# Performance work log

Hardware: AMD Instinct MI355X
Metric: run time of the kernel (lower is better)

Reference implementation:

```python
import jax, jax.numpy as jnp
import numpy as np

N_CODES = 1024
CODE_DIM = 64
COMMITMENT_WEIGHT = 0.5
DECAY = 0.99
EPSILON = 1e-05
TEMP = 1.0


def setup_inputs() -> dict:
    key = jax.random.key(0)
    k_z, k_e = jax.random.split(key)
    z = jax.random.normal(k_z, (8, 16384, CODE_DIM), dtype=jnp.float32)
    # xavier_uniform init for embedding [n_codes, code_dim]
    limit = float(np.sqrt(6.0 / (N_CODES + CODE_DIM)))
    embedding = jax.random.uniform(k_e, (N_CODES, CODE_DIM), dtype=jnp.float32,
                                   minval=-limit, maxval=limit)
    ema_cluster_size = jnp.zeros((N_CODES,), dtype=jnp.float32)
    ema_w = embedding.copy()
    return {"z": z, "embedding": embedding,
            "ema_cluster_size": ema_cluster_size, "ema_w": ema_w}


def reference(z, embedding, ema_cluster_size, ema_w):
    lead_shape = z.shape[:-1]
    zf = z.reshape(-1, z.shape[-1])  # [N, D]
    # squared-euclidean distances: ||z||^2 + ||e||^2 - 2 z e^T  -> [N, n_codes]
    d = (jnp.sum(zf * zf, axis=-1, keepdims=True)
         + jnp.sum(embedding * embedding, axis=-1)
         - 2.0 * (zf @ embedding.T)) / TEMP
    idx = jnp.argmin(d, axis=-1)  # [N]
    z_q_f = embedding[idx]        # [N, D]

    # --- EMA codebook update (no-grad buffer math) ---
    ones = jnp.ones_like(idx, dtype=zf.dtype)
    cluster_size = jax.ops.segment_sum(ones, idx, num_segments=N_CODES)      # one_hot.sum(0)
    new_ecs = ema_cluster_size * DECAY + (1.0 - DECAY) * cluster_size
    n = jnp.sum(new_ecs)
    cs = jnp.clip((new_ecs + EPSILON) / (n + N_CODES * EPSILON) * n, 0.01)
    dw = jax.ops.segment_sum(zf, idx, num_segments=N_CODES)                  # one_hot.T @ z
    new_ema_w = ema_w * DECAY + (1.0 - DECAY) * dw
    new_embedding = new_ema_w / cs[:, None]

    # --- losses (straight-through) ---
    z_q = z_q_f.reshape(z.shape)
    commitment_loss = jnp.mean((jax.lax.stop_gradient(z_q) - z) ** 2)
    codebook_loss = jnp.mean((z_q - jax.lax.stop_gradient(z)) ** 2)
    loss = commitment_loss * COMMITMENT_WEIGHT + codebook_loss
    z_q_st = z + jax.lax.stop_gradient(z_q - z)

    # --- perplexity (no-grad) ---
    avg_probs = cluster_size / jnp.sum(cluster_size)
    avg_probs = jnp.clip(avg_probs, 1e-10)
    avg_probs = avg_probs / jnp.sum(avg_probs)
    perplexity = jnp.exp(-jnp.sum(avg_probs * jnp.log(avg_probs)))

    encoding_indices = idx.reshape(lead_shape)
    return (z_q_st, encoding_indices, loss, perplexity,
            new_embedding, new_ecs, new_ema_w)
```

## Files before the change

kernel.cpp:

```cpp
#include <hip/hip_runtime.h>
#include <hip/hip_bf16.h>
#include <math.h>

#define N_ROWS   131072
#define DIMS     64
#define NCODES   1024
#define DECAY    0.99f
#define EPSF     1e-5f
#define BAND     2e-3f

#define OFF_ZQ    0
#define OFF_IDX   8388608
#define OFF_LOSS  8519680
#define OFF_PERP  8519681
#define OFF_EMB   8519682
#define OFF_ECS   8585218
#define OFF_EMAW  8586242

typedef unsigned int uint;
typedef short bf16x8 __attribute__((ext_vector_type(8)));
typedef float f32x4  __attribute__((ext_vector_type(4)));

__device__ __forceinline__ float atomic_add_f32(float* p, float v) {
  return __hip_atomic_fetch_add(p, v, __ATOMIC_RELAXED, __HIP_MEMORY_SCOPE_AGENT);
}

__device__ __forceinline__ unsigned short bf16_rne(float f) {
  uint u = __float_as_uint(f);
  uint r = u + 0x7fffu + ((u >> 16) & 1u);
  return (unsigned short)(r >> 16);
}
__device__ __forceinline__ float bf16_f32(unsigned short h) {
  return __uint_as_float(((uint)h) << 16);
}

__device__ __forceinline__ float np_pairwise64_sq(const float* v) {
#pragma clang fp contract(off)
  float r[8];
#pragma unroll
  for (int j = 0; j < 8; ++j) r[j] = v[j] * v[j];
#pragma unroll
  for (int i = 8; i < 64; i += 8)
#pragma unroll
    for (int j = 0; j < 8; ++j) r[j] += v[i + j] * v[i + j];
  return ((r[0] + r[1]) + (r[2] + r[3])) + ((r[4] + r[5]) + (r[6] + r[7]));
}

__global__ __launch_bounds__(256) void k0m(const float* __restrict__ emb,
                                           float* __restrict__ ee,
                                           uint* __restrict__ cluster,
                                           uint* __restrict__ cnt,
                                           bf16x8* __restrict__ bsplit,
                                           float* __restrict__ dw) {
  int T = blockIdx.x;
  int t = threadIdx.x;
  int gid = T * 256 + t;
  for (int i = gid; i < NCODES * DIMS; i += 16384) dw[i] = 0.0f;

  int l = t & 63;
  int slot = t >> 6;
  int ktile = slot >> 1, split = slot & 1;
  int code = T * 16 + (l & 15);
  int k0 = ktile * 32 + ((l >> 4) << 3);
  const float* ep = emb + (size_t)code * DIMS + k0;
  float4 fa = *(const float4*)ep;
  float4 fb = *(const float4*)(ep + 4);
  float fs[8] = {fa.x, fa.y, fa.z, fa.w, fb.x, fb.y, fb.z, fb.w};
  bf16x8 v;
#pragma unroll
  for (int i = 0; i < 8; ++i) {
    unsigned short h = bf16_rne(fs[i]);
    if (split == 0) v[i] = (short)h;
    else            v[i] = (short)bf16_rne(fs[i] - bf16_f32(h));
  }
  bsplit[(size_t)((T * 2 + ktile) * 2 + split) * 64 + l] = v;

  if (t < 16) {
    int c = T * 16 + t;
    float ev[DIMS];
    const float4* e4 = (const float4*)(emb + (size_t)c * DIMS);
#pragma unroll
    for (int i = 0; i < 16; ++i) {
      float4 w = e4[i];
      ev[4*i] = w.x; ev[4*i+1] = w.y; ev[4*i+2] = w.z; ev[4*i+3] = w.w;
    }
    ee[c] = np_pairwise64_sq(ev);
  } else if (t < 32) {
    cluster[T * 16 + (t - 16)] = 0u;
  }
  if (T == 0 && t == 32) *cnt = 0u;
}

__global__ __launch_bounds__(256) void k1_mfma(const float* __restrict__ z,
                                               const bf16x8* __restrict__ bsplit,
                                               const float* __restrict__ ee,
                                               int* __restrict__ idx_out,
                                               float* __restrict__ idx_f_out,
                                               uint* __restrict__ cluster,
                                               uint* __restrict__ cnt,
                                               uint* __restrict__ list) {
  __shared__ bf16x8 btile[4 * 64];
  __shared__ float  eel[NCODES];
  int t = threadIdx.x;
  int l = t & 63;
  int w = t >> 6;
  int rowbase = blockIdx.x * 64 + w * 16;
  int arow = rowbase + (l & 15);
  int kq = (l >> 4) << 3;
  int col = l & 15;

  for (int i = t; i < NCODES; i += 256) eel[i] = ee[i];

  bf16x8 ahi[2], ami[2];
#pragma unroll
  for (int t2 = 0; t2 < 2; ++t2) {
    const float* zp = z + (size_t)arow * DIMS + t2 * 32 + kq;
    float4 fa = *(const float4*)zp;
    float4 fb = *(const float4*)(zp + 4);
    float fs[8] = {fa.x, fa.y, fa.z, fa.w, fb.x, fb.y, fb.z, fb.w};
#pragma unroll
    for (int i = 0; i < 8; ++i) {
      unsigned short h = bf16_rne(fs[i]);
      float m = fs[i] - bf16_f32(h);
      ahi[t2][i] = (short)bf16_rne(-2.0f * fs[i]);
      ami[t2][i] = (short)bf16_rne(-2.0f * m);
    }
  }

  float best[4]  = {3.4e38f, 3.4e38f, 3.4e38f, 3.4e38f};
  float second[4] = {3.4e38f, 3.4e38f, 3.4e38f, 3.4e38f};
  int   bidx[4] = {0, 0, 0, 0};

  bf16x8 vpre = bsplit[(size_t)(0 * 4 + w) * 64 + l];

  for (int T = 0; T < 64; ++T) {
    __syncthreads();
    btile[w * 64 + l] = vpre;
    if (T < 63) vpre = bsplit[(size_t)((T + 1) * 4 + w) * 64 + l];
    __syncthreads();

    int code = T * 16 + col;
    float eeT = eel[code];
    bf16x8 bhi0 = btile[0 * 64 + l];
    bf16x8 bmi0 = btile[1 * 64 + l];
    bf16x8 bhi1 = btile[2 * 64 + l];
    bf16x8 bmi1 = btile[3 * 64 + l];

    f32x4 acc = {eeT, eeT, eeT, eeT};
    acc = __builtin_amdgcn_mfma_f32_16x16x32_bf16(ahi[0], bhi0, acc, 0, 0, 0);
    acc = __builtin_amdgcn_mfma_f32_16x16x32_bf16(ahi[1], bhi1, acc, 0, 0, 0);
    acc = __builtin_amdgcn_mfma_f32_16x16x32_bf16(ahi[0], bmi0, acc, 0, 0, 0);
    acc = __builtin_amdgcn_mfma_f32_16x16x32_bf16(ahi[1], bmi1, acc, 0, 0, 0);
    acc = __builtin_amdgcn_mfma_f32_16x16x32_bf16(ami[0], bhi0, acc, 0, 0, 0);
    acc = __builtin_amdgcn_mfma_f32_16x16x32_bf16(ami[1], bhi1, acc, 0, 0, 0);

#pragma unroll
    for (int j = 0; j < 4; ++j) {
      float s = acc[j];
      bool lt = s < best[j];
      second[j] = lt ? best[j] : fminf(second[j], s);
      best[j]   = lt ? s : best[j];
      bidx[j]   = lt ? code : bidx[j];
    }
  }

#pragma unroll
  for (int m = 1; m < 16; m <<= 1) {
#pragma unroll
    for (int j = 0; j < 4; ++j) {
      float ob = __shfl_xor(best[j], m, 64);
      float os = __shfl_xor(second[j], m, 64);
      int   oi = __shfl_xor(bidx[j], m, 64);
      if (ob < best[j]) {
        second[j] = fminf(os, best[j]);
        best[j] = ob; bidx[j] = oi;
      } else if (ob == best[j]) {
        bidx[j] = min(bidx[j], oi);
        second[j] = fminf(second[j], fminf(os, ob));
      } else {
        second[j] = fminf(second[j], ob);
      }
    }
  }

  if (col == 0) {
#pragma unroll
    for (int j = 0; j < 4; ++j) {
      int r = rowbase + ((l >> 4) << 2) + j;
      idx_out[r] = bidx[j];
      idx_f_out[r] = (float)bidx[j];
      atomicAdd(&cluster[bidx[j]], 1u);
      if (second[j] - best[j] < BAND) {
        uint p = atomicAdd(cnt, 1u);
        list[p] = (uint)r;
      }
    }
  }
}

__global__ __launch_bounds__(256) void k2_recheck(const float* __restrict__ z,
                                                  const float* __restrict__ emb,
                                                  const float* __restrict__ ee,
                                                  const uint* __restrict__ cnt,
                                                  const uint* __restrict__ list,
                                                  int* __restrict__ idx_out,
                                                  float* __restrict__ idx_f_out,
                                                  uint* __restrict__ cluster) {
#pragma clang fp contract(off)
  __shared__ float zrow[DIMS];
  __shared__ float rv[256];
  __shared__ int   ri[256];
  int t = threadIdx.x;
  uint n = *cnt;
  for (uint i = blockIdx.x; i < n; i += gridDim.x) {
    uint row = list[i];
    __syncthreads();
    if (t < 16)
      ((float4*)zrow)[t] = ((const float4*)(z + (size_t)row * DIMS))[t];
    __syncthreads();
    float zz = np_pairwise64_sq(zrow);
    float best = 3.4e38f; int bi = 0;
#pragma unroll
    for (int k4 = 0; k4 < 4; ++k4) {
      int c = t * 4 + k4;
      const float* e = emb + (size_t)c * DIMS;
      float a = 0.f;
      for (int k = 0; k < DIMS; ++k) a = fmaf(zrow[k], e[k], a);
      float d = fmaf(-2.0f, a, zz + ee[c]);
      if (d < best) { best = d; bi = c; }
    }
    rv[t] = best; ri[t] = bi;
    __syncthreads();
    for (int s = 128; s > 0; s >>= 1) {
      if (t < s) {
        float ov = rv[t + s]; int oi = ri[t + s];
        if (ov < rv[t] || (ov == rv[t] && oi < ri[t])) { rv[t] = ov; ri[t] = oi; }
      }
      __syncthreads();
    }
    if (t == 0) {
      int old = idx_out[row];
      if (ri[0] != old) {
        atomicSub(&cluster[old], 1u);
        atomicAdd(&cluster[ri[0]], 1u);
        idx_out[row] = ri[0];
        idx_f_out[row] = (float)ri[0];
      }
    }
  }
}

__global__ __launch_bounds__(256) void kp(const uint* __restrict__ cluster,
                                          const float* __restrict__ ecs_in,
                                          uint* __restrict__ starts,
                                          uint* __restrict__ cursor,
                                          float* __restrict__ csb,
                                          float* __restrict__ out) {
  __shared__ uint a[256], b[256];
  __shared__ double red[256];
  int t = threadIdx.x;

  uint c0 = cluster[t*4+0], c1 = cluster[t*4+1], c2 = cluster[t*4+2], c3 = cluster[t*4+3];
  uint s4 = c0 + c1 + c2 + c3;
  a[t] = s4;
  __syncthreads();
  uint* src = a; uint* dst = b;
  for (int off = 1; off < 256; off <<= 1) {
    dst[t] = src[t] + ((t >= off) ? src[t - off] : 0u);
    __syncthreads();
    uint* tmp = src; src = dst; dst = tmp;
  }
  uint base = (t > 0) ? src[t-1] : 0u;
  uint p0 = base, p1 = p0 + c0, p2 = p1 + c1, p3 = p2 + c2;
  starts[t*4+0] = p0; starts[t*4+1] = p1; starts[t*4+2] = p2; starts[t*4+3] = p3;
  cursor[t*4+0] = p0; cursor[t*4+1] = p1; cursor[t*4+2] = p2; cursor[t*4+3] = p3;
  if (t == 255) starts[NCODES] = src[255];
  __syncthreads();

  double nloc = 0.0, aloc = 0.0, bloc = 0.0;
  for (int c = t; c < NCODES; c += 256) {
    float cntf = (float)cluster[c];
    float ne = ecs_in[c] * DECAY + (1.0f - DECAY) * cntf;
    out[OFF_ECS + c] = ne;
    nloc += (double)ne;
    double p = (double)cntf / (double)N_ROWS;
    double pc = p < 1e-10 ? 1e-10 : p;
    bloc += pc;
    aloc += pc * log(pc);
  }

  red[t] = nloc; __syncthreads();
  for (int s = 128; s > 0; s >>= 1) { if (t < s) red[t] += red[t + s]; __syncthreads(); }
  double n = red[0]; __syncthreads();

  red[t] = bloc; __syncthreads();
  for (int s = 128; s > 0; s >>= 1) { if (t < s) red[t] += red[t + s]; __syncthreads(); }
  double B = red[0]; __syncthreads();

  red[t] = aloc; __syncthreads();
  for (int s = 128; s > 0; s >>= 1) { if (t < s) red[t] += red[t + s]; __syncthreads(); }
  double A = red[0]; __syncthreads();

  if (t == 0) {
    double ent = -(A / B - log(B));
    out[OFF_PERP] = (float)exp(ent);
  }

  float nf = (float)n;
  for (int c = t; c < NCODES; c += 256) {
    float ne = out[OFF_ECS + c];
    float cs = ((ne + EPSF) / (nf + (float)NCODES * EPSF)) * nf;
    csb[c] = cs < 0.01f ? 0.01f : cs;
  }
}

__global__ __launch_bounds__(256) void k3c_scatter(const int* __restrict__ idx,
                                                   uint* __restrict__ cursor,
                                                   uint* __restrict__ rowids,
                                                   int* __restrict__ codes) {
  int row = blockIdx.x * 256 + threadIdx.x;
  int code = idx[row];
  uint pos = atomicAdd(&cursor[code], 1u);
  rowids[pos] = (uint)row;
  codes[pos] = code;
}

__global__ __launch_bounds__(256) void k3d_fused(const float* __restrict__ z,
                                                 const float* __restrict__ emb,
                                                 const uint* __restrict__ rowids,
                                                 const int* __restrict__ codes,
                                                 float* __restrict__ out_zq,
                                                 float* __restrict__ dw,
                                                 double* __restrict__ sqpart) {
  __shared__ double accd[4];
  int lane = threadIdx.x & 63, w = threadIdx.x >> 6;
  int base = blockIdx.x * 128 + w * 32;

  int cur = codes[base];
  float acc = 0.f;
  double ds = 0.0;
  for (int i = 0; i < 32; ++i) {
    int p = base + i;
    uint r = rowids[p];
    int c = codes[p];
    if (c != cur) {
      atomic_add_f32(&dw[cur * DIMS + lane], acc);
      acc = 0.f; cur = c;
    }
    float zv = z[(size_t)r * DIMS + lane];
    float ev = emb[c * DIMS + lane];
    float d = ev - zv;
    float o = zv + d;
    out_zq[(size_t)r * DIMS + lane] = o;
    acc += zv;
    ds += (double)(d * d);
  }
  atomic_add_f32(&dw[cur * DIMS + lane], acc);

#pragma unroll
  for (int o2 = 32; o2 > 0; o2 >>= 1) ds += __shfl_down(ds, o2, 64);
  if (lane == 0) accd[w] = ds;
  __syncthreads();
  if (threadIdx.x == 0)
    sqpart[blockIdx.x] = (accd[0] + accd[1]) + (accd[2] + accd[3]);
}

__global__ __launch_bounds__(256) void k4b_emb(const float* __restrict__ emaw_in,
                                               const float* __restrict__ dw,
                                               const float* __restrict__ csb,
                                               const double* __restrict__ sqpart,
                                               float* __restrict__ out) {
  int i = blockIdx.x * 256 + threadIdx.x;
  int c = i >> 6;
  float nw = emaw_in[i] * DECAY + (1.0f - DECAY) * dw[i];
  out[OFF_EMAW + i] = nw;
  out[OFF_EMB + i] = nw / csb[c];

  if (blockIdx.x == 0) {
    __shared__ double red[256];
    int t = threadIdx.x;
    double sloc = 0.0;
    for (int k = t; k < 1024; k += 256) sloc += sqpart[k];
    red[t] = sloc; __syncthreads();
    for (int s = 128; s > 0; s >>= 1) { if (t < s) red[t] += red[t + s]; __syncthreads(); }
    if (t == 0) {
      double M = red[0] / (double)((size_t)N_ROWS * DIMS);
      out[OFF_LOSS] = (float)(1.5 * M);
    }
  }
}

extern "C" void kernel_launch(void* const* d_in, const int* in_sizes, int n_in,
                              void* d_out, int out_size, void* d_ws, size_t ws_size,
                              hipStream_t stream) {
  const float* z    = (const float*)d_in[0];
  const float* emb  = (const float*)d_in[1];
  const float* ecs  = (const float*)d_in[2];
  const float* emaw = (const float*)d_in[3];
  float* out = (float*)d_out;

  char* ws = (char*)d_ws;
  uint*   cnt    = (uint*)   (ws + 0);
  int*    idxw   = (int*)    (ws + 16);
  uint*   clus   = (uint*)   (ws + 524304);
  float*  dw     = (float*)  (ws + 528416);
  float*  ee     = (float*)  (ws + 790560);
  float*  csb    = (float*)  (ws + 794656);
  uint*   starts = (uint*)   (ws + 798752);
  uint*   cursor = (uint*)   (ws + 806944);
  uint*   rowids = (uint*)   (ws + 811040);
  bf16x8* bsplit = (bf16x8*) (ws + 1335328);
  uint*   rlist  = (uint*)   (ws + 1597472);
  double* sqpart = (double*) (ws + 1597472);
  int*    codes  = (int*)    (ws + 2121760);

  k0m<<<64, 256, 0, stream>>>(emb, ee, clus, cnt, bsplit, dw);
  k1_mfma<<<N_ROWS / 64, 256, 0, stream>>>(z, bsplit, ee, idxw, out + OFF_IDX,
                                           clus, cnt, rlist);
  k2_recheck<<<1024, 256, 0, stream>>>(z, emb, ee, cnt, rlist, idxw,
                                       out + OFF_IDX, clus);
  kp<<<1, 256, 0, stream>>>(clus, ecs, starts, cursor, csb, out);
  k3c_scatter<<<N_ROWS / 256, 256, 0, stream>>>(idxw, cursor, rowids, codes);
  k3d_fused<<<N_ROWS / 128, 256, 0, stream>>>(z, emb, rowids, codes,
                                              out + OFF_ZQ, dw, sqpart);
  k4b_emb<<<256, 256, 0, stream>>>(emaw, dw, csb, sqpart, out);
}
```

Measured before the change: 195.4 us.

## Fuse z_q output and loss partials into the MFMA argmin kernel

Moves the straight-through z_q write and the squared-error loss partial sums out of the sorted-order dw kernel and into the argmin kernel, where z rows are read coalesced by block. Rows whose index changes during the exact recheck get their z_q rewritten and a loss correction term recorded, which the final kernel adds back in. The dw kernel now only gathers z. The argmin loop also stages two code tiles per barrier pair, halving the number of synchronisations. This removes the scattered z_q writes but adds an extra z read in the argmin kernel and a correction path.

```diff
diff --git a/kernel.cpp b/kernel.cpp
--- a/kernel.cpp
+++ b/kernel.cpp
@@ -92,15 +92,20 @@
 }
 
 __global__ __launch_bounds__(256) void k1_mfma(const float* __restrict__ z,
+                                               const float* __restrict__ emb,
                                                const bf16x8* __restrict__ bsplit,
                                                const float* __restrict__ ee,
                                                int* __restrict__ idx_out,
                                                float* __restrict__ idx_f_out,
+                                               float* __restrict__ out_zq,
+                                               double* __restrict__ sqpart,
                                                uint* __restrict__ cluster,
                                                uint* __restrict__ cnt,
                                                uint* __restrict__ list) {
-  __shared__ bf16x8 btile[4 * 64];
+  __shared__ bf16x8 btile[2][256];
   __shared__ float  eel[NCODES];
+  __shared__ int    sidx[64];
+  __shared__ double wred[4];
   int t = threadIdx.x;
   int l = t & 63;
   int w = t >> 6;
@@ -131,36 +136,44 @@
   float second[4] = {3.4e38f, 3.4e38f, 3.4e38f, 3.4e38f};
   int   bidx[4] = {0, 0, 0, 0};
 
-  bf16x8 vpre = bsplit[(size_t)(0 * 4 + w) * 64 + l];
-
-  for (int T = 0; T < 64; ++T) {
-    __syncthreads();
-    btile[w * 64 + l] = vpre;
-    if (T < 63) vpre = bsplit[(size_t)((T + 1) * 4 + w) * 64 + l];
-    __syncthreads();
-
-    int code = T * 16 + col;
-    float eeT = eel[code];
-    bf16x8 bhi0 = btile[0 * 64 + l];
-    bf16x8 bmi0 = btile[1 * 64 + l];
-    bf16x8 bhi1 = btile[2 * 64 + l];
-    bf16x8 bmi1 = btile[3 * 64 + l];
-
-    f32x4 acc = {eeT, eeT, eeT, eeT};
-    acc = __builtin_amdgcn_mfma_f32_16x16x32_bf16(ahi[0], bhi0, acc, 0, 0, 0);
-    acc = __builtin_amdgcn_mfma_f32_16x16x32_bf16(ahi[1], bhi1, acc, 0, 0, 0);
-    acc = __builtin_amdgcn_mfma_f32_16x16x32_bf16(ahi[0], bmi0, acc, 0, 0, 0);
-    acc = __builtin_amdgcn_mfma_f32_16x16x32_bf16(ahi[1], bmi1, acc, 0, 0, 0);
-    acc = __builtin_amdgcn_mfma_f32_16x16x32_bf16(ami[0], bhi0, acc, 0, 0, 0);
-    acc = __builtin_amdgcn_mfma_f32_16x16x32_bf16(ami[1], bhi1, acc, 0, 0, 0);
-
-#pragma unroll
-    for (int j = 0; j < 4; ++j) {
-      float s = acc[j];
-      bool lt = s < best[j];
-      second[j] = lt ? best[j] : fminf(second[j], s);
-      best[j]   = lt ? s : best[j];
-      bidx[j]   = lt ? code : bidx[j];
+  bf16x8 vp0 = bsplit[(size_t)(0 * 4 + w) * 64 + l];
+  bf16x8 vp1 = bsplit[(size_t)(1 * 4 + w) * 64 + l];
+
+  for (int T = 0; T < 64; T += 2) {
+    __syncthreads();
+    btile[0][w * 64 + l] = vp0;
+    btile[1][w * 64 + l] = vp1;
+    __syncthreads();
+    if (T + 2 < 64) {
+      vp0 = bsplit[(size_t)((T + 2) * 4 + w) * 64 + l];
+      vp1 = bsplit[(size_t)((T + 3) * 4 + w) * 64 + l];
+    }
+
+#pragma unroll
+    for (int u = 0; u < 2; ++u) {
+      int code = (T + u) * 16 + col;
+      float eeT = eel[code];
+      bf16x8 bhi0 = btile[u][0 * 64 + l];
+      bf16x8 bmi0 = btile[u][1 * 64 + l];
+      bf16x8 bhi1 = btile[u][2 * 64 + l];
+      bf16x8 bmi1 = btile[u][3 * 64 + l];
+
+      f32x4 acc = {eeT, eeT, eeT, eeT};
+      acc = __builtin_amdgcn_mfma_f32_16x16x32_bf16(ahi[0], bhi0, acc, 0, 0, 0);
+      acc = __builtin_amdgcn_mfma_f32_16x16x32_bf16(ahi[1], bhi1, acc, 0, 0, 0);
+      acc = __builtin_amdgcn_mfma_f32_16x16x32_bf16(ahi[0], bmi0, acc, 0, 0, 0);
+      acc = __builtin_amdgcn_mfma_f32_16x16x32_bf16(ahi[1], bmi1, acc, 0, 0, 0);
+      acc = __builtin_amdgcn_mfma_f32_16x16x32_bf16(ami[0], bhi0, acc, 0, 0, 0);
+      acc = __builtin_amdgcn_mfma_f32_16x16x32_bf16(ami[1], bhi1, acc, 0, 0, 0);
+
+#pragma unroll
+      for (int j = 0; j < 4; ++j) {
+        float s = acc[j];
+        bool lt = s < best[j];
+        second[j] = lt ? best[j] : fminf(second[j], s);
+        best[j]   = lt ? s : best[j];
+        bidx[j]   = lt ? code : bidx[j];
+      }
     }
   }
 
@@ -186,7 +199,9 @@
   if (col == 0) {
 #pragma unroll
     for (int j = 0; j < 4; ++j) {
-      int r = rowbase + ((l >> 4) << 2) + j;
+      int lrow = w * 16 + ((l >> 4) << 2) + j;
+      int r = blockIdx.x * 64 + lrow;
+      sidx[lrow] = bidx[j];
       idx_out[r] = bidx[j];
       idx_f_out[r] = (float)bidx[j];
       atomicAdd(&cluster[bidx[j]], 1u);
@@ -196,6 +211,32 @@
       }
     }
   }
+  __syncthreads();
+
+  double ds = 0.0;
+  const float4* z4 = (const float4*)z;
+  const float4* e4 = (const float4*)emb;
+  float4* zq4 = (float4*)out_zq;
+  int blockrow = blockIdx.x * 64;
+#pragma unroll
+  for (int p = 0; p < 4; ++p) {
+    int f = t + p * 256;
+    int lrow = f >> 4, d4 = f & 15;
+    int code = sidx[lrow];
+    float4 zv = z4[(size_t)(blockrow + lrow) * 16 + d4];
+    float4 ev = e4[code * 16 + d4];
+    float dx = ev.x - zv.x, dy = ev.y - zv.y, dz = ev.z - zv.z, dw_ = ev.w - zv.w;
+    float4 o;
+    o.x = zv.x + dx; o.y = zv.y + dy; o.z = zv.z + dz; o.w = zv.w + dw_;
+    zq4[(size_t)(blockrow + lrow) * 16 + d4] = o;
+    float ss = dx * dx + dy * dy + dz * dz + dw_ * dw_;
+    ds += (double)ss;
+  }
+#pragma unroll
+  for (int o2 = 32; o2 > 0; o2 >>= 1) ds += __shfl_down(ds, o2, 64);
+  if (l == 0) wred[w] = ds;
+  __syncthreads();
+  if (t == 0) sqpart[blockIdx.x] = (wred[0] + wred[1]) + (wred[2] + wred[3]);
 }
 
 __global__ __launch_bounds__(256) void k2_recheck(const float* __restrict__ z,
@@ -205,13 +246,20 @@
                                                   const uint* __restrict__ list,
                                                   int* __restrict__ idx_out,
                                                   float* __restrict__ idx_f_out,
-                                                  uint* __restrict__ cluster) {
+                                                  float* __restrict__ out_zq,
+                                                  uint* __restrict__ cluster,
+                                                  double* __restrict__ corr) {
 #pragma clang fp contract(off)
   __shared__ float zrow[DIMS];
   __shared__ float rv[256];
   __shared__ int   ri[256];
+  __shared__ int   schg, sold, snew;
   int t = threadIdx.x;
   uint n = *cnt;
+  double corrAcc = 0.0;
+  const float4* e4 = (const float4*)emb;
+  float4* zq4 = (float4*)out_zq;
+
   for (uint i = blockIdx.x; i < n; i += gridDim.x) {
     uint row = list[i];
     __syncthreads();
@@ -245,9 +293,32 @@
         atomicAdd(&cluster[ri[0]], 1u);
         idx_out[row] = ri[0];
         idx_f_out[row] = (float)ri[0];
+        schg = 1; sold = old; snew = ri[0];
+      } else {
+        schg = 0;
       }
     }
-  }
+    __syncthreads();
+    if (schg && t < 16) {
+      float4 zv = make_float4(zrow[t*4], zrow[t*4+1], zrow[t*4+2], zrow[t*4+3]);
+      float4 en = e4[snew * 16 + t];
+      float4 eo = e4[sold * 16 + t];
+      float dxn = en.x - zv.x, dyn = en.y - zv.y, dzn = en.z - zv.z, dwn = en.w - zv.w;
+      float4 o;
+      o.x = zv.x + dxn; o.y = zv.y + dyn; o.z = zv.z + dzn; o.w = zv.w + dwn;
+      zq4[(size_t)row * 16 + t] = o;
+      float ssn = dxn * dxn + dyn * dyn + dzn * dzn + dwn * dwn;
+      float dxo = eo.x - zv.x, dyo = eo.y - zv.y, dzo = eo.z - zv.z, dwo = eo.w - zv.w;
+      float sso = dxo * dxo + dyo * dyo + dzo * dzo + dwo * dwo;
+      double cl = (double)ssn - (double)sso;
+      cl += __shfl_xor(cl, 1, 64);
+      cl += __shfl_xor(cl, 2, 64);
+      cl += __shfl_xor(cl, 4, 64);
+      cl += __shfl_xor(cl, 8, 64);
+      if (t == 0) corrAcc += cl;
+    }
+  }
+  if (t == 0) corr[blockIdx.x] = corrAcc;
 }
 
 __global__ __launch_bounds__(256) void kp(const uint* __restrict__ cluster,
@@ -325,20 +396,15 @@
   codes[pos] = code;
 }
 
-__global__ __launch_bounds__(256) void k3d_fused(const float* __restrict__ z,
-                                                 const float* __restrict__ emb,
-                                                 const uint* __restrict__ rowids,
-                                                 const int* __restrict__ codes,
-                                                 float* __restrict__ out_zq,
-                                                 float* __restrict__ dw,
-                                                 double* __restrict__ sqpart) {
-  __shared__ double accd[4];
+__global__ __launch_bounds__(256) void k3d_dw(const float* __restrict__ z,
+                                              const uint* __restrict__ rowids,
+                                              const int* __restrict__ codes,
+                                              float* __restrict__ dw) {
   int lane = threadIdx.x & 63, w = threadIdx.x >> 6;
   int base = blockIdx.x * 128 + w * 32;
 
   int cur = codes[base];
   float acc = 0.f;
-  double ds = 0.0;
   for (int i = 0; i < 32; ++i) {
     int p = base + i;
     uint r = rowids[p];
@@ -347,28 +413,16 @@
       atomic_add_f32(&dw[cur * DIMS + lane], acc);
       acc = 0.f; cur = c;
     }
-    float zv = z[(size_t)r * DIMS + lane];
-    float ev = emb[c * DIMS + lane];
-    float d = ev - zv;
-    float o = zv + d;
-    out_zq[(size_t)r * DIMS + lane] = o;
-    acc += zv;
-    ds += (double)(d * d);
+    acc += z[(size_t)r * DIMS + lane];
   }
   atomic_add_f32(&dw[cur * DIMS + lane], acc);
-
-#pragma unroll
-  for (int o2 = 32; o2 > 0; o2 >>= 1) ds += __shfl_down(ds, o2, 64);
-  if (lane == 0) accd[w] = ds;
-  __syncthreads();
-  if (threadIdx.x == 0)
-    sqpart[blockIdx.x] = (accd[0] + accd[1]) + (accd[2] + accd[3]);
 }
 
 __global__ __launch_bounds__(256) void k4b_emb(const float* __restrict__ emaw_in,
                                                const float* __restrict__ dw,
                                                const float* __restrict__ csb,
                                                const double* __restrict__ sqpart,
+                                               const double* __restrict__ corr,
                                                float* __restrict__ out) {
   int i = blockIdx.x * 256 + threadIdx.x;
   int c = i >> 6;
@@ -380,7 +434,8 @@
     __shared__ double red[256];
     int t = threadIdx.x;
     double sloc = 0.0;
-    for (int k = t; k < 1024; k += 256) sloc += sqpart[k];
+    for (int k = t; k < 2048; k += 256) sloc += sqpart[k];
+    for (int k = t; k < 1024; k += 256) sloc += corr[k];
     red[t] = sloc; __syncthreads();
     for (int s = 128; s > 0; s >>= 1) { if (t < s) red[t] += red[t + s]; __syncthreads(); }
     if (t == 0) {
@@ -411,17 +466,18 @@
   uint*   rowids = (uint*)   (ws + 811040);
   bf16x8* bsplit = (bf16x8*) (ws + 1335328);
   uint*   rlist  = (uint*)   (ws + 1597472);
-  double* sqpart = (double*) (ws + 1597472);
   int*    codes  = (int*)    (ws + 2121760);
+  double* sqpart = (double*) (ws + 2646048);
+  double* corr   = (double*) (ws + 2662432);
 
   k0m<<<64, 256, 0, stream>>>(emb, ee, clus, cnt, bsplit, dw);
-  k1_mfma<<<N_ROWS / 64, 256, 0, stream>>>(z, bsplit, ee, idxw, out + OFF_IDX,
-                                           clus, cnt, rlist);
+  k1_mfma<<<N_ROWS / 64, 256, 0, stream>>>(z, emb, bsplit, ee, idxw,
+                                           out + OFF_IDX, out + OFF_ZQ,
+                                           sqpart, clus, cnt, rlist);
   k2_recheck<<<1024, 256, 0, stream>>>(z, emb, ee, cnt, rlist, idxw,
-                                       out + OFF_IDX, clus);
+                                       out + OFF_IDX, out + OFF_ZQ, clus, corr);
   kp<<<1, 256, 0, stream>>>(clus, ecs, starts, cursor, csb, out);
   k3c_scatter<<<N_ROWS / 256, 256, 0, stream>>>(idxw, cursor, rowids, codes);
-  k3d_fused<<<N_ROWS / 128, 256, 0, stream>>>(z, emb, rowids, codes,
-                                              out + OFF_ZQ, dw, sqpart);
-  k4b_emb<<<256, 256, 0, stream>>>(emaw, dw, csb, sqpart, out);
-}
+  k3d_dw<<<N_ROWS / 128, 256, 0, stream>>>(z, rowids, codes, dw);
+  k4b_emb<<<256, 256, 0, stream>>>(emaw, dw, csb, sqpart, corr, out);
+}
```

Result: faster. 191.3 us (median of 3 runs) (-2.1%).
